# Optimization experiments

Hardware: AMD Instinct MI355X
Metric: run time of the kernel (lower is better)

Reference implementation:

```python
import jax, jax.numpy as jnp
import numpy as np

B, D, H, L, T = 4096, 256, 512, 2, 45


def _lstm_cell(x, h, c, W_ih, W_hh, b_ih, b_hh):
    # PyTorch LSTM gate order: i, f, g, o
    gates = x @ W_ih + h @ W_hh + b_ih + b_hh  # [B, 4H]
    i, f, g, o = jnp.split(gates, 4, axis=-1)
    i = jax.nn.sigmoid(i)
    f = jax.nn.sigmoid(f)
    g = jnp.tanh(g)
    o = jax.nn.sigmoid(o)
    c_new = f * c + i * g
    h_new = o * jnp.tanh(c_new)
    return h_new, c_new


def setup_inputs() -> dict:
    key = jax.random.key(0)
    ks = jax.random.split(key, 32)
    s = 0.02
    inp = {
        "encoder_feat": jax.random.normal(ks[0], (B, D), jnp.float32),
        "context": jax.random.normal(ks[1], (B, D), jnp.float32),
        "initial_intent": jax.random.uniform(ks[2], (B, 1), jnp.float32),
        # hidden/cell init linears: d_model -> H*L (stored [in, out])
        "Wh_init": jax.random.normal(ks[3], (D, H * L), jnp.float32) * s,
        "bh_init": jnp.zeros((H * L,), jnp.float32),
        "Wc_init": jax.random.normal(ks[4], (D, H * L), jnp.float32) * s,
        "bc_init": jnp.zeros((H * L,), jnp.float32),
        # LSTM layer 0: input size 1 + d_model
        "W_ih0": jax.random.normal(ks[5], (1 + D, 4 * H), jnp.float32) * s,
        "W_hh0": jax.random.normal(ks[6], (H, 4 * H), jnp.float32) * s,
        "b_ih0": jnp.zeros((4 * H,), jnp.float32),
        "b_hh0": jnp.zeros((4 * H,), jnp.float32),
        # LSTM layer 1: input size H
        "W_ih1": jax.random.normal(ks[7], (H, 4 * H), jnp.float32) * s,
        "W_hh1": jax.random.normal(ks[8], (H, 4 * H), jnp.float32) * s,
        "b_ih1": jnp.zeros((4 * H,), jnp.float32),
        "b_hh1": jnp.zeros((4 * H,), jnp.float32),
        # output_proj: H -> 32 -> 1
        "Wo1": jax.random.normal(ks[9], (H, 32), jnp.float32) * s,
        "bo1": jnp.zeros((32,), jnp.float32),
        "Wo2": jax.random.normal(ks[10], (32, 1), jnp.float32) * s,
        "bo2": jnp.zeros((1,), jnp.float32),
        # global_intent_head: H -> 32 -> 1
        "Wg1": jax.random.normal(ks[11], (H, 32), jnp.float32) * s,
        "bg1": jnp.zeros((32,), jnp.float32),
        "Wg2": jax.random.normal(ks[12], (32, 1), jnp.float32) * s,
        "bg2": jnp.zeros((1,), jnp.float32),
    }
    return inp


def reference(encoder_feat, context, initial_intent,
              Wh_init, bh_init, Wc_init, bc_init,
              W_ih0, W_hh0, b_ih0, b_hh0,
              W_ih1, W_hh1, b_ih1, b_hh1,
              Wo1, bo1, Wo2, bo2, Wg1, bg1, Wg2, bg2):
    # init hidden/cell: [B, L*H] -> [B, L, H]; layer-major slices
    h_init = (encoder_feat @ Wh_init + bh_init).reshape(B, L, H)
    c_init = (encoder_feat @ Wc_init + bc_init).reshape(B, L, H)
    h0, h1 = h_init[:, 0], h_init[:, 1]
    c0, c1 = c_init[:, 0], c_init[:, 1]

    def step(carry, _):
        h0, c0, h1, c1, intent = carry
        x = jnp.concatenate([intent, context], axis=-1)  # [B, 1+D]
        h0n, c0n = _lstm_cell(x, h0, c0, W_ih0, W_hh0, b_ih0, b_hh0)
        h1n, c1n = _lstm_cell(h0n, h1, c1, W_ih1, W_hh1, b_ih1, b_hh1)
        logit = jax.nn.relu(h1n @ Wo1 + bo1) @ Wo2 + bo2  # [B, 1]
        intent_new = jax.nn.sigmoid(logit)
        return (h0n, c0n, h1n, c1n, intent_new), intent_new

    carry0 = (h0, c0, h1, c1, initial_intent)
    (h0, c0, h1, c1, _), ys = jax.lax.scan(step, carry0, None, length=T)
    step_intents = jnp.transpose(ys, (1, 0, 2))  # [B, T, 1]
    global_logit = jax.nn.relu(h1 @ Wg1 + bg1) @ Wg2 + bg2
    global_intent = jax.nn.sigmoid(global_logit)  # [B, 1]
    return step_intents, global_intent
```

## Files before the change

### kernel.cpp

```cpp
#include <hip/hip_runtime.h>
#include <hip/hip_bf16.h>

#define Bsz 4096
#define Dsz 256
#define Hsz 512
#define Tsz 45

typedef __attribute__((ext_vector_type(8))) short short8;
typedef __attribute__((ext_vector_type(4))) float f32x4;
using bf16 = __hip_bfloat16;

__device__ __forceinline__ float sigf(float x)   { return 1.0f / (1.0f + __expf(-x)); }
__device__ __forceinline__ float tanhft(float x) { return 1.0f - 2.0f / (__expf(2.0f * x) + 1.0f); }

__device__ __forceinline__ void gload16(const void* g, void* l) {
    __builtin_amdgcn_global_load_lds((const __attribute__((address_space(1))) void*)g,
                                     (__attribute__((address_space(3))) void*)l, 16, 0, 0);
}

__global__ void k_conv(const float* __restrict__ ef,   const float* __restrict__ ctx,
                       const float* __restrict__ Whi,  const float* __restrict__ Wci,
                       const float* __restrict__ Wih0, const float* __restrict__ Whh0,
                       const float* __restrict__ Wih1, const float* __restrict__ Whh1,
                       const float* __restrict__ Wo1,  const float* __restrict__ Wg1,
                       bf16* __restrict__ efb,  bf16* __restrict__ ctxb,
                       bf16* __restrict__ Wit,  bf16* __restrict__ Wt0,
                       bf16* __restrict__ Wt1,  bf16* __restrict__ Wo1t,
                       bf16* __restrict__ Wg1t)
{
    size_t tid = (size_t)blockIdx.x * blockDim.x + threadIdx.x;
    size_t gsz = (size_t)gridDim.x * blockDim.x;
    for (size_t i = tid; i < (size_t)Bsz * Dsz; i += gsz) {
        efb[i]  = __float2bfloat16(ef[i]);
        ctxb[i] = __float2bfloat16(ctx[i]);
    }
    for (size_t i = tid; i < 2048ull * 512; i += gsz) {
        size_t n = i >> 9, k = i & 511;
        Wt0[i] = __float2bfloat16(Whh0[k * 2048 + n]);
    }
    for (size_t i = tid; i < 2048ull * 1024; i += gsz) {
        size_t n = i >> 10, k = i & 1023;
        Wt1[i] = __float2bfloat16(k < 512 ? Wih1[k * 2048 + n] : Whh1[(k - 512) * 2048 + n]);
    }
    for (size_t i = tid; i < 32ull * 512; i += gsz) {
        size_t c = i >> 9, k = i & 511;
        Wo1t[i] = __float2bfloat16(Wo1[k * 32 + c]);
        Wg1t[i] = __float2bfloat16(Wg1[k * 32 + c]);
    }
    for (size_t i = tid; i < 4096ull * 256; i += gsz) {
        size_t n = i >> 8, k = i & 255;
        float v = (n < 1024) ? Whi[k * 1024 + n]
                : (n < 2048) ? Wci[k * 1024 + (n - 1024)]
                             : Wih0[(1 + k) * 2048 + (n - 2048)];
        Wit[i] = __float2bfloat16(v);
    }
}

__global__ void __launch_bounds__(256)
k_init(const bf16* __restrict__ efb, const bf16* __restrict__ ctxb,
       const bf16* __restrict__ Wit,
       const float* __restrict__ bh,  const float* __restrict__ bc,
       const float* __restrict__ bi0, const float* __restrict__ bh0,
       bf16* __restrict__ h0, bf16* __restrict__ h1,
       float* __restrict__ c0, float* __restrict__ c1,
       bf16* __restrict__ ctxg)
{
    const int t = threadIdx.x, lane = t & 63, w = t >> 6;
    const int wr = w >> 1, wc = w & 1;
    const int lq = lane >> 4, ln = lane & 15;
    const int m0 = blockIdx.x * 128, n0 = blockIdx.y * 64;
    const bf16* A = (n0 < 2048) ? efb : ctxb;

    f32x4 zero = {0.f, 0.f, 0.f, 0.f};
    f32x4 acc[4][2];
#pragma unroll
    for (int r = 0; r < 4; ++r)
#pragma unroll
        for (int c = 0; c < 2; ++c) acc[r][c] = zero;

    for (int k0 = 0; k0 < 256; k0 += 32) {
        short8 af[4];
#pragma unroll
        for (int r = 0; r < 4; ++r)
            af[r] = *(const short8*)(A + (size_t)(m0 + wr * 64 + r * 16 + ln) * 256 + k0 + lq * 8);
#pragma unroll
        for (int c = 0; c < 2; ++c) {
            short8 bv = *(const short8*)(Wit + (size_t)(n0 + wc * 32 + c * 16 + ln) * 256 + k0 + lq * 8);
#pragma unroll
            for (int r = 0; r < 4; ++r)
                acc[r][c] = __builtin_amdgcn_mfma_f32_16x16x32_bf16(af[r], bv, acc[r][c], 0, 0, 0);
        }
    }
#pragma unroll
    for (int r = 0; r < 4; ++r)
#pragma unroll
        for (int c = 0; c < 2; ++c)
#pragma unroll
            for (int e = 0; e < 4; ++e) {
                int b = m0 + wr * 64 + r * 16 + lq * 4 + e;
                int n = n0 + wc * 32 + c * 16 + ln;
                float v = acc[r][c][e];
                if (n < 1024) {
                    v += bh[n];
                    if (n < 512) h0[(size_t)b * 512 + n]       = __float2bfloat16(v);
                    else         h1[(size_t)b * 512 + n - 512] = __float2bfloat16(v);
                } else if (n < 2048) {
                    int m = n - 1024; v += bc[m];
                    if (m < 512) c0[(size_t)b * 512 + m]       = v;
                    else         c1[(size_t)b * 512 + m - 512] = v;
                } else {
                    int j = n - 2048;
                    ctxg[(size_t)b * 2048 + j] = __float2bfloat16(v + bi0[j] + bh0[j]);
                }
            }
}

template <int L0>
__global__ void __launch_bounds__(256)
k_gates(const bf16* __restrict__ hA, const bf16* __restrict__ hB,
        const bf16* __restrict__ Wt,
        const bf16* __restrict__ ctxg, const float* __restrict__ intent,
        const float* __restrict__ w0row,
        const float* __restrict__ b1, const float* __restrict__ b2,
        float* __restrict__ cbuf, bf16* __restrict__ hout)
{
    constexpr int KW = L0 ? 512 : 1024;
    __shared__ __align__(16) bf16 As[128 * 32];
    __shared__ __align__(16) bf16 Bs[4 * 32 * 32];
    const int t = threadIdx.x;
    const int lane = t & 63, w = t >> 6;
    const int wr = w >> 1, wc = w & 1;
    const int lq = lane >> 4, ln = lane & 15;
    const int m0 = blockIdx.x * 128, j0 = blockIdx.y * 32;

    f32x4 zero = {0.f, 0.f, 0.f, 0.f};
    f32x4 acc[4][4];
#pragma unroll
    for (int g = 0; g < 4; ++g)
#pragma unroll
        for (int r = 0; r < 4; ++r) acc[g][r] = zero;

    for (int k0 = 0; k0 < KW; k0 += 32) {
        __syncthreads();
#pragma unroll
        for (int i = 0; i < 2; ++i) {
            int chunk = i * 256 + t;
            int row = chunk >> 2, kc = chunk & 3;
            int kk = k0 + (kc ^ ((row >> 2) & 3)) * 8;
            const bf16* src;
            if (L0) src = hA + (size_t)(m0 + row) * Hsz + kk;
            else    src = (k0 < 512) ? hA + (size_t)(m0 + row) * Hsz + kk
                                     : hB + (size_t)(m0 + row) * Hsz + (kk - 512);
            gload16(src, (char*)As + (size_t)(i * 256 + w * 64) * 16);
        }
#pragma unroll
        for (int i = 0; i < 2; ++i) {
            int chunk = i * 256 + t;
            int g = chunk >> 7, rem = chunk & 127;
            int n = rem >> 2, kc = rem & 3;
            int kk = k0 + (kc ^ ((n >> 2) & 3)) * 8;
            const bf16* src = Wt + (size_t)(g * 512 + j0 + n) * KW + kk;
            gload16(src, (char*)Bs + (size_t)(i * 256 + w * 64) * 16);
        }
        __syncthreads();

        short8 af[4];
#pragma unroll
        for (int r = 0; r < 4; ++r) {
            int row = wr * 64 + r * 16 + ln;
            int c = lq ^ ((row >> 2) & 3);
            af[r] = *(const short8*)(As + row * 32 + c * 8);
        }
#pragma unroll
        for (int g = 0; g < 4; ++g) {
            int n = wc * 16 + ln;
            int c = lq ^ ((n >> 2) & 3);
            short8 bv = *(const short8*)(Bs + (g * 32 + n) * 32 + c * 8);
#pragma unroll
            for (int r = 0; r < 4; ++r)
                acc[g][r] = __builtin_amdgcn_mfma_f32_16x16x32_bf16(af[r], bv, acc[g][r], 0, 0, 0);
        }
    }

    const int jl = j0 + wc * 16 + ln;
    float addc[4];
#pragma unroll
    for (int g = 0; g < 4; ++g)
        addc[g] = L0 ? w0row[g * 512 + jl] : (b1[g * 512 + jl] + b2[g * 512 + jl]);

#pragma unroll
    for (int r = 0; r < 4; ++r)
#pragma unroll
        for (int e = 0; e < 4; ++e) {
            int b = m0 + wr * 64 + r * 16 + lq * 4 + e;
            float pre[4];
#pragma unroll
            for (int g = 0; g < 4; ++g) pre[g] = acc[g][r][e];
            if (L0) {
                float it = intent[b];
#pragma unroll
                for (int g = 0; g < 4; ++g)
                    pre[g] += __bfloat162float(ctxg[(size_t)b * 2048 + g * 512 + jl]) + it * addc[g];
            } else {
#pragma unroll
                for (int g = 0; g < 4; ++g) pre[g] += addc[g];
            }
            float ig = sigf(pre[0]), fg = sigf(pre[1]);
            float gg = tanhft(pre[2]), og = sigf(pre[3]);
            size_t idx = (size_t)b * Hsz + jl;
            float cn = fg * cbuf[idx] + ig * gg;
            cbuf[idx] = cn;
            hout[idx] = __float2bfloat16(og * tanhft(cn));
        }
}

__global__ void __launch_bounds__(256)
k_intent(const bf16* __restrict__ h, const bf16* __restrict__ W1t,
         const float* __restrict__ bias1, const float* __restrict__ W2,
         const float* __restrict__ bias2,
         float* __restrict__ outp, int ostride, float* __restrict__ iws)
{
    const int t = threadIdx.x, lane = t & 63, w = t >> 6;
    const int wr = w >> 1, wc = w & 1;
    const int lq = lane >> 4, ln = lane & 15;
    const int m0 = blockIdx.x * 128;
    __shared__ float part[128][2];

    f32x4 zero = {0.f, 0.f, 0.f, 0.f};
    f32x4 acc[4];
#pragma unroll
    for (int r = 0; r < 4; ++r) acc[r] = zero;

    for (int k0 = 0; k0 < 512; k0 += 32) {
        short8 bv = *(const short8*)(W1t + (size_t)(wc * 16 + ln) * 512 + k0 + lq * 8);
#pragma unroll
        for (int r = 0; r < 4; ++r) {
            short8 av = *(const short8*)(h + (size_t)(m0 + wr * 64 + r * 16 + ln) * 512 + k0 + lq * 8);
            acc[r] = __builtin_amdgcn_mfma_f32_16x16x32_bf16(av, bv, acc[r], 0, 0, 0);
        }
    }
    int col = wc * 16 + ln;
    float b1v = bias1[col], w2v = W2[col];
#pragma unroll
    for (int r = 0; r < 4; ++r)
#pragma unroll
        for (int e = 0; e < 4; ++e) {
            float v = fmaxf(acc[r][e] + b1v, 0.f) * w2v;
            v += __shfl_xor(v, 1);
            v += __shfl_xor(v, 2);
            v += __shfl_xor(v, 4);
            v += __shfl_xor(v, 8);
            if (ln == 0) part[wr * 64 + r * 16 + lq * 4 + e][wc] = v;
        }
    __syncthreads();
    if (t < 128) {
        int b = m0 + t;
        float p = sigf(part[t][0] + part[t][1] + bias2[0]);
        outp[(size_t)b * ostride] = p;
        if (iws) iws[b] = p;
    }
}

extern "C" void kernel_launch(void* const* d_in, const int* in_sizes, int n_in,
                              void* d_out, int out_size, void* d_ws, size_t ws_size,
                              hipStream_t stream)
{
    const float* ef   = (const float*)d_in[0];
    const float* ctx  = (const float*)d_in[1];
    const float* ii   = (const float*)d_in[2];
    const float* Whi  = (const float*)d_in[3];
    const float* bh   = (const float*)d_in[4];
    const float* Wci  = (const float*)d_in[5];
    const float* bc   = (const float*)d_in[6];
    const float* Wih0 = (const float*)d_in[7];
    const float* Whh0 = (const float*)d_in[8];
    const float* bi0  = (const float*)d_in[9];
    const float* bh0  = (const float*)d_in[10];
    const float* Wih1 = (const float*)d_in[11];
    const float* Whh1 = (const float*)d_in[12];
    const float* bi1  = (const float*)d_in[13];
    const float* bh1  = (const float*)d_in[14];
    const float* Wo1  = (const float*)d_in[15];
    const float* bo1  = (const float*)d_in[16];
    const float* Wo2  = (const float*)d_in[17];
    const float* bo2  = (const float*)d_in[18];
    const float* Wg1  = (const float*)d_in[19];
    const float* bg1  = (const float*)d_in[20];
    const float* Wg2  = (const float*)d_in[21];
    const float* bg2  = (const float*)d_in[22];
    float* out = (float*)d_out;

    char* ws = (char*)d_ws;
    size_t off = 0;
    auto take = [&](size_t bytes) -> char* {
        char* p = ws + off;
        off += (bytes + 255) & ~(size_t)255;
        return p;
    };
    bf16* Wt0    = (bf16*)take(2048ull * 512 * 2);
    bf16* Wt1    = (bf16*)take(2048ull * 1024 * 2);
    bf16* Wo1t   = (bf16*)take(32ull * 512 * 2);
    bf16* Wg1t   = (bf16*)take(32ull * 512 * 2);
    bf16* Wit    = (bf16*)take(4096ull * 256 * 2);
    bf16* efb    = (bf16*)take((size_t)Bsz * Dsz * 2);
    bf16* ctxb   = (bf16*)take((size_t)Bsz * Dsz * 2);
    bf16* h0b[2] = {(bf16*)take((size_t)Bsz * Hsz * 2), (bf16*)take((size_t)Bsz * Hsz * 2)};
    bf16* h1b[2] = {(bf16*)take((size_t)Bsz * Hsz * 2), (bf16*)take((size_t)Bsz * Hsz * 2)};
    float* c0    = (float*)take((size_t)Bsz * Hsz * 4);
    float* c1    = (float*)take((size_t)Bsz * Hsz * 4);
    bf16* ctxg   = (bf16*)take((size_t)Bsz * 2048 * 2);
    float* iws   = (float*)take((size_t)Bsz * 4);
    (void)ws_size; (void)in_sizes; (void)n_in; (void)out_size;

    k_conv<<<2048, 256, 0, stream>>>(ef, ctx, Whi, Wci, Wih0, Whh0, Wih1, Whh1, Wo1, Wg1,
                                     efb, ctxb, Wit, Wt0, Wt1, Wo1t, Wg1t);
    k_init<<<dim3(32, 64), 256, 0, stream>>>(efb, ctxb, Wit, bh, bc, bi0, bh0,
                                             h0b[0], h1b[0], c0, c1, ctxg);
    for (int s = 0; s < Tsz; ++s) {
        int p = s & 1;
        const float* it = (s == 0) ? ii : iws;
        k_gates<1><<<dim3(32, 16), 256, 0, stream>>>(h0b[p], nullptr, Wt0, ctxg, it, Wih0,
                                                     nullptr, nullptr, c0, h0b[1 - p]);
        k_gates<0><<<dim3(32, 16), 256, 0, stream>>>(h0b[1 - p], h1b[p], Wt1, nullptr, nullptr,
                                                     nullptr, bi1, bh1, c1, h1b[1 - p]);
        k_intent<<<32, 256, 0, stream>>>(h1b[1 - p], Wo1t, bo1, Wo2, bo2, out + s, Tsz, iws);
    }
    k_intent<<<32, 256, 0, stream>>>(h1b[1], Wg1t, bg1, Wg2, bg2, out + (size_t)Bsz * Tsz, 1, nullptr);
}
```

Baseline: 2.831 ms.

## Fuse intent head into layer-0 gates and double-buffer LDS with wider K tiles

Removes the per-step k_intent launch by recomputing the intent MLP inside each layer-0 gates block from the previous h1, with only blockIdx.x==0 blocks writing the output. The gates GEMM now stages 64-wide K tiles into double-buffered LDS with an 8-slot XOR swizzle, so the next tile's loads overlap the current tile's MFMAs. The grid is transposed and launch bounds raised to 2 blocks per CU. ctxg is stored gate-interleaved so each thread reads its four gate values in one vector load. The cost is that the intent head is recomputed redundantly in every column block and LDS use grows to 64 KB per block.

```diff
diff --git a/kernel.cpp b/kernel.cpp
--- a/kernel.cpp
+++ b/kernel.cpp
@@ -8,10 +8,12 @@
 
 typedef __attribute__((ext_vector_type(8))) short short8;
 typedef __attribute__((ext_vector_type(4))) float f32x4;
+typedef __attribute__((ext_vector_type(4))) unsigned short us4;
 using bf16 = __hip_bfloat16;
 
 __device__ __forceinline__ float sigf(float x)   { return 1.0f / (1.0f + __expf(-x)); }
 __device__ __forceinline__ float tanhft(float x) { return 1.0f - 2.0f / (__expf(2.0f * x) + 1.0f); }
+__device__ __forceinline__ float b2f(unsigned short u) { return __uint_as_float((unsigned)u << 16); }
 
 __device__ __forceinline__ void gload16(const void* g, void* l) {
     __builtin_amdgcn_global_load_lds((const __attribute__((address_space(1))) void*)g,
@@ -110,28 +112,137 @@
                     else         c1[(size_t)b * 512 + m - 512] = v;
                 } else {
                     int j = n - 2048;
-                    ctxg[(size_t)b * 2048 + j] = __float2bfloat16(v + bi0[j] + bh0[j]);
+                    ctxg[(size_t)b * 2048 + (j & 511) * 4 + (j >> 9)] =
+                        __float2bfloat16(v + bi0[j] + bh0[j]);
                 }
             }
 }
 
+__device__ __forceinline__ void intent_head(
+    const bf16* __restrict__ h, const bf16* __restrict__ W1t,
+    const float* __restrict__ b1, const float* __restrict__ W2, float b2s,
+    int m0, float* sitp, float* outp, int ostride)
+{
+    const int t = threadIdx.x, lane = t & 63, w = t >> 6;
+    const int lq = lane >> 4, ln = lane & 15;
+    f32x4 zero = {0.f, 0.f, 0.f, 0.f};
+    f32x4 acc[2][2];
+#pragma unroll
+    for (int r = 0; r < 2; ++r)
+#pragma unroll
+        for (int c = 0; c < 2; ++c) acc[r][c] = zero;
+
+#pragma unroll
+    for (int k0 = 0; k0 < 512; k0 += 32) {
+        short8 av[2], bv[2];
+#pragma unroll
+        for (int r = 0; r < 2; ++r)
+            av[r] = *(const short8*)(h + (size_t)(m0 + w * 32 + r * 16 + ln) * 512 + k0 + lq * 8);
+#pragma unroll
+        for (int c = 0; c < 2; ++c)
+            bv[c] = *(const short8*)(W1t + (size_t)(c * 16 + ln) * 512 + k0 + lq * 8);
+#pragma unroll
+        for (int r = 0; r < 2; ++r)
+#pragma unroll
+            for (int c = 0; c < 2; ++c)
+                acc[r][c] = __builtin_amdgcn_mfma_f32_16x16x32_bf16(av[r], bv[c], acc[r][c], 0, 0, 0);
+    }
+#pragma unroll
+    for (int r = 0; r < 2; ++r)
+#pragma unroll
+        for (int e = 0; e < 4; ++e) {
+            float v = 0.f;
+#pragma unroll
+            for (int c = 0; c < 2; ++c) {
+                int col = c * 16 + ln;
+                v += fmaxf(acc[r][c][e] + b1[col], 0.f) * W2[col];
+            }
+            v += __shfl_xor(v, 1);
+            v += __shfl_xor(v, 2);
+            v += __shfl_xor(v, 4);
+            v += __shfl_xor(v, 8);
+            int row = w * 32 + r * 16 + lq * 4 + e;
+            if (ln == 0) {
+                float p = sigf(v + b2s);
+                if (sitp) sitp[row] = p;
+                if (outp) outp[(size_t)(m0 + row) * ostride] = p;
+            }
+        }
+}
+
 template <int L0>
-__global__ void __launch_bounds__(256)
+__device__ __forceinline__ void stage(const bf16* __restrict__ hA, const bf16* __restrict__ hB,
+                                      const bf16* __restrict__ Wt,
+                                      int m0, int j0, int k0, bf16* Ab, bf16* Bb, int t)
+{
+    constexpr int KW = L0 ? 512 : 1024;
+#pragma unroll
+    for (int i = 0; i < 4; ++i) {
+        int f = i * 256 + t;
+        int row = f >> 3, slot = f & 7;
+        int kk = k0 + ((slot ^ (row & 7)) << 3);
+        const bf16* src;
+        if (L0) src = hA + (size_t)(m0 + row) * Hsz + kk;
+        else    src = (kk < 512) ? hA + (size_t)(m0 + row) * Hsz + kk
+                                 : hB + (size_t)(m0 + row) * Hsz + (kk - 512);
+        gload16(src, (char*)Ab + (size_t)f * 16);
+    }
+#pragma unroll
+    for (int i = 0; i < 4; ++i) {
+        int f = i * 256 + t;
+        int brow = f >> 3, slot = f & 7;
+        int g = brow >> 5, n = brow & 31;
+        int kc = slot ^ (brow & 7);
+        gload16(Wt + (size_t)(g * 512 + j0 + n) * KW + k0 + kc * 8, (char*)Bb + (size_t)f * 16);
+    }
+}
+
+template <int L0>
+__global__ void __launch_bounds__(256, 2)
 k_gates(const bf16* __restrict__ hA, const bf16* __restrict__ hB,
         const bf16* __restrict__ Wt,
-        const bf16* __restrict__ ctxg, const float* __restrict__ intent,
+        const bf16* __restrict__ ctxg, const float* __restrict__ ii,
+        const bf16* __restrict__ h1prev,
         const float* __restrict__ w0row,
         const float* __restrict__ b1, const float* __restrict__ b2,
-        float* __restrict__ cbuf, bf16* __restrict__ hout)
+        const bf16* __restrict__ Wo1t, const float* __restrict__ bo1,
+        const float* __restrict__ Wo2, const float* __restrict__ bo2,
+        float* __restrict__ cbuf, bf16* __restrict__ hout,
+        float* __restrict__ outp, int step)
 {
     constexpr int KW = L0 ? 512 : 1024;
-    __shared__ __align__(16) bf16 As[128 * 32];
-    __shared__ __align__(16) bf16 Bs[4 * 32 * 32];
-    const int t = threadIdx.x;
-    const int lane = t & 63, w = t >> 6;
-    const int wr = w >> 1, wc = w & 1;
-    const int lq = lane >> 4, ln = lane & 15;
-    const int m0 = blockIdx.x * 128, j0 = blockIdx.y * 32;
+    constexpr int NT = KW / 64;
+    __shared__ __align__(16) char lds[65536];
+    bf16* A0 = (bf16*)lds;
+    bf16* A1 = (bf16*)(lds + 16384);
+    bf16* B0 = (bf16*)(lds + 32768);
+    bf16* B1 = (bf16*)(lds + 49152);
+    float* sitp = (float*)(lds + 49152);
+
+    const int t = threadIdx.x, lane = t & 63, w = t >> 6;
+    const int wr = w >> 1, wc = w & 1, lq = lane >> 4, ln = lane & 15;
+    const int j0 = blockIdx.x * 32, m0 = blockIdx.y * 128;
+
+    stage<L0>(hA, hB, Wt, m0, j0, 0, A0, B0, t);
+
+    float sreg[16];
+    if (L0) {
+        if (step == 0) {
+            if (t < 128) sitp[t] = ii[m0 + t];
+        } else {
+            intent_head(h1prev, Wo1t, bo1, Wo2, bo2[0], m0, sitp,
+                        (blockIdx.x == 0) ? outp + (step - 1) : nullptr, Tsz);
+        }
+        __syncthreads();
+#pragma unroll
+        for (int r = 0; r < 4; ++r)
+#pragma unroll
+            for (int e = 0; e < 4; ++e)
+                sreg[r * 4 + e] = sitp[wr * 64 + r * 16 + lq * 4 + e];
+        __syncthreads();
+    } else {
+        __syncthreads();
+    }
 
     f32x4 zero = {0.f, 0.f, 0.f, 0.f};
     f32x4 acc[4][4];
@@ -140,46 +251,35 @@
 #pragma unroll
         for (int r = 0; r < 4; ++r) acc[g][r] = zero;
 
-    for (int k0 = 0; k0 < KW; k0 += 32) {
-        __syncthreads();
-#pragma unroll
-        for (int i = 0; i < 2; ++i) {
-            int chunk = i * 256 + t;
-            int row = chunk >> 2, kc = chunk & 3;
-            int kk = k0 + (kc ^ ((row >> 2) & 3)) * 8;
-            const bf16* src;
-            if (L0) src = hA + (size_t)(m0 + row) * Hsz + kk;
-            else    src = (k0 < 512) ? hA + (size_t)(m0 + row) * Hsz + kk
-                                     : hB + (size_t)(m0 + row) * Hsz + (kk - 512);
-            gload16(src, (char*)As + (size_t)(i * 256 + w * 64) * 16);
-        }
-#pragma unroll
-        for (int i = 0; i < 2; ++i) {
-            int chunk = i * 256 + t;
-            int g = chunk >> 7, rem = chunk & 127;
-            int n = rem >> 2, kc = rem & 3;
-            int kk = k0 + (kc ^ ((n >> 2) & 3)) * 8;
-            const bf16* src = Wt + (size_t)(g * 512 + j0 + n) * KW + kk;
-            gload16(src, (char*)Bs + (size_t)(i * 256 + w * 64) * 16);
-        }
-        __syncthreads();
-
-        short8 af[4];
-#pragma unroll
-        for (int r = 0; r < 4; ++r) {
-            int row = wr * 64 + r * 16 + ln;
-            int c = lq ^ ((row >> 2) & 3);
-            af[r] = *(const short8*)(As + row * 32 + c * 8);
-        }
-#pragma unroll
-        for (int g = 0; g < 4; ++g) {
-            int n = wc * 16 + ln;
-            int c = lq ^ ((n >> 2) & 3);
-            short8 bv = *(const short8*)(Bs + (g * 32 + n) * 32 + c * 8);
-#pragma unroll
-            for (int r = 0; r < 4; ++r)
-                acc[g][r] = __builtin_amdgcn_mfma_f32_16x16x32_bf16(af[r], bv, acc[g][r], 0, 0, 0);
-        }
+#pragma unroll 2
+    for (int kt = 0; kt < NT; ++kt) {
+        if (kt + 1 < NT)
+            stage<L0>(hA, hB, Wt, m0, j0, (kt + 1) * 64,
+                      (kt & 1) ? A0 : A1, (kt & 1) ? B0 : B1, t);
+        const bf16* Ab = (kt & 1) ? A1 : A0;
+        const bf16* Bb = (kt & 1) ? B1 : B0;
+#pragma unroll
+        for (int kk2 = 0; kk2 < 2; ++kk2) {
+            short8 af[4], bfr[4];
+#pragma unroll
+            for (int r = 0; r < 4; ++r) {
+                int row = wr * 64 + r * 16 + ln;
+                int slot = (kk2 * 4 + lq) ^ (row & 7);
+                af[r] = *(const short8*)(Ab + ((size_t)row * 8 + slot) * 8);
+            }
+#pragma unroll
+            for (int g = 0; g < 4; ++g) {
+                int brow = g * 32 + wc * 16 + ln;
+                int slot = (kk2 * 4 + lq) ^ (brow & 7);
+                bfr[g] = *(const short8*)(Bb + ((size_t)brow * 8 + slot) * 8);
+            }
+#pragma unroll
+            for (int g = 0; g < 4; ++g)
+#pragma unroll
+                for (int r = 0; r < 4; ++r)
+                    acc[g][r] = __builtin_amdgcn_mfma_f32_16x16x32_bf16(af[r], bfr[g], acc[g][r], 0, 0, 0);
+        }
+        if (kt + 1 < NT) __syncthreads();
     }
 
     const int jl = j0 + wc * 16 + ln;
@@ -197,10 +297,10 @@
 #pragma unroll
             for (int g = 0; g < 4; ++g) pre[g] = acc[g][r][e];
             if (L0) {
-                float it = intent[b];
-#pragma unroll
-                for (int g = 0; g < 4; ++g)
-                    pre[g] += __bfloat162float(ctxg[(size_t)b * 2048 + g * 512 + jl]) + it * addc[g];
+                float it = sreg[r * 4 + e];
+                us4 cg = *(const us4*)((const unsigned short*)ctxg + (size_t)b * 2048 + jl * 4);
+#pragma unroll
+                for (int g = 0; g < 4; ++g) pre[g] += b2f(cg[g]) + it * addc[g];
             } else {
 #pragma unroll
                 for (int g = 0; g < 4; ++g) pre[g] += addc[g];
@@ -218,47 +318,9 @@
 k_intent(const bf16* __restrict__ h, const bf16* __restrict__ W1t,
          const float* __restrict__ bias1, const float* __restrict__ W2,
          const float* __restrict__ bias2,
-         float* __restrict__ outp, int ostride, float* __restrict__ iws)
-{
-    const int t = threadIdx.x, lane = t & 63, w = t >> 6;
-    const int wr = w >> 1, wc = w & 1;
-    const int lq = lane >> 4, ln = lane & 15;
-    const int m0 = blockIdx.x * 128;
-    __shared__ float part[128][2];
-
-    f32x4 zero = {0.f, 0.f, 0.f, 0.f};
-    f32x4 acc[4];
-#pragma unroll
-    for (int r = 0; r < 4; ++r) acc[r] = zero;
-
-    for (int k0 = 0; k0 < 512; k0 += 32) {
-        short8 bv = *(const short8*)(W1t + (size_t)(wc * 16 + ln) * 512 + k0 + lq * 8);
-#pragma unroll
-        for (int r = 0; r < 4; ++r) {
-            short8 av = *(const short8*)(h + (size_t)(m0 + wr * 64 + r * 16 + ln) * 512 + k0 + lq * 8);
-            acc[r] = __builtin_amdgcn_mfma_f32_16x16x32_bf16(av, bv, acc[r], 0, 0, 0);
-        }
-    }
-    int col = wc * 16 + ln;
-    float b1v = bias1[col], w2v = W2[col];
-#pragma unroll
-    for (int r = 0; r < 4; ++r)
-#pragma unroll
-        for (int e = 0; e < 4; ++e) {
-            float v = fmaxf(acc[r][e] + b1v, 0.f) * w2v;
-            v += __shfl_xor(v, 1);
-            v += __shfl_xor(v, 2);
-            v += __shfl_xor(v, 4);
-            v += __shfl_xor(v, 8);
-            if (ln == 0) part[wr * 64 + r * 16 + lq * 4 + e][wc] = v;
-        }
-    __syncthreads();
-    if (t < 128) {
-        int b = m0 + t;
-        float p = sigf(part[t][0] + part[t][1] + bias2[0]);
-        outp[(size_t)b * ostride] = p;
-        if (iws) iws[b] = p;
-    }
+         float* __restrict__ outp, int ostride)
+{
+    intent_head(h, W1t, bias1, W2, bias2[0], blockIdx.x * 128, nullptr, outp, ostride);
 }
 
 extern "C" void kernel_launch(void* const* d_in, const int* in_sizes, int n_in,
@@ -293,9 +355,9 @@
     char* ws = (char*)d_ws;
     size_t off = 0;
     auto take = [&](size_t bytes) -> char* {
-        char* p = ws + off;
+        char* pp = ws + off;
         off += (bytes + 255) & ~(size_t)255;
-        return p;
+        return pp;
     };
     bf16* Wt0    = (bf16*)take(2048ull * 512 * 2);
     bf16* Wt1    = (bf16*)take(2048ull * 1024 * 2);
@@ -304,26 +366,33 @@
     bf16* Wit    = (bf16*)take(4096ull * 256 * 2);
     bf16* efb    = (bf16*)take((size_t)Bsz * Dsz * 2);
     bf16* ctxb   = (bf16*)take((size_t)Bsz * Dsz * 2);
-    bf16* h0b[2] = {(bf16*)take((size_t)Bsz * Hsz * 2), (bf16*)take((size_t)Bsz * Hsz * 2)};
-    bf16* h1b[2] = {(bf16*)take((size_t)Bsz * Hsz * 2), (bf16*)take((size_t)Bsz * Hsz * 2)};
+    bf16* h0x    = (bf16*)take((size_t)Bsz * Hsz * 2);
+    bf16* h0y    = (bf16*)take((size_t)Bsz * Hsz * 2);
+    bf16* h1x    = (bf16*)take((size_t)Bsz * Hsz * 2);
+    bf16* h1y    = (bf16*)take((size_t)Bsz * Hsz * 2);
     float* c0    = (float*)take((size_t)Bsz * Hsz * 4);
     float* c1    = (float*)take((size_t)Bsz * Hsz * 4);
     bf16* ctxg   = (bf16*)take((size_t)Bsz * 2048 * 2);
-    float* iws   = (float*)take((size_t)Bsz * 4);
     (void)ws_size; (void)in_sizes; (void)n_in; (void)out_size;
 
     k_conv<<<2048, 256, 0, stream>>>(ef, ctx, Whi, Wci, Wih0, Whh0, Wih1, Whh1, Wo1, Wg1,
                                      efb, ctxb, Wit, Wt0, Wt1, Wo1t, Wg1t);
     k_init<<<dim3(32, 64), 256, 0, stream>>>(efb, ctxb, Wit, bh, bc, bi0, bh0,
-                                             h0b[0], h1b[0], c0, c1, ctxg);
+                                             h0x, h1x, c0, c1, ctxg);
+
     for (int s = 0; s < Tsz; ++s) {
         int p = s & 1;
-        const float* it = (s == 0) ? ii : iws;
-        k_gates<1><<<dim3(32, 16), 256, 0, stream>>>(h0b[p], nullptr, Wt0, ctxg, it, Wih0,
-                                                     nullptr, nullptr, c0, h0b[1 - p]);
-        k_gates<0><<<dim3(32, 16), 256, 0, stream>>>(h0b[1 - p], h1b[p], Wt1, nullptr, nullptr,
-                                                     nullptr, bi1, bh1, c1, h1b[1 - p]);
-        k_intent<<<32, 256, 0, stream>>>(h1b[1 - p], Wo1t, bo1, Wo2, bo2, out + s, Tsz, iws);
-    }
-    k_intent<<<32, 256, 0, stream>>>(h1b[1], Wg1t, bg1, Wg2, bg2, out + (size_t)Bsz * Tsz, 1, nullptr);
-}
+        const bf16* h0in  = p ? h0y : h0x;
+        bf16*       h0out = p ? h0x : h0y;
+        const bf16* h1in  = p ? h1y : h1x;
+        bf16*       h1out = p ? h1x : h1y;
+        k_gates<1><<<dim3(16, 32), 256, 0, stream>>>(
+            h0in, nullptr, Wt0, ctxg, ii, h1in, Wih0, nullptr, nullptr,
+            Wo1t, bo1, Wo2, bo2, c0, h0out, out, s);
+        k_gates<0><<<dim3(16, 32), 256, 0, stream>>>(
+            h0out, h1in, Wt1, nullptr, nullptr, nullptr, nullptr, bi1, bh1,
+            nullptr, nullptr, nullptr, nullptr, c1, h1out, nullptr, s);
+    }
+    k_intent<<<32, 256, 0, stream>>>(h1y, Wo1t, bo1, Wo2, bo2, out + 44, Tsz);
+    k_intent<<<32, 256, 0, stream>>>(h1y, Wg1t, bg1, Wg2, bg2, out + (size_t)Bsz * Tsz, 1);
+}
```

After: 2.757 ms. 2.6% less time.
